# Optimization experiments

Measured on AMD Instinct MI355X. Metric: run time of the kernel, lower is better.

Reference implementation:

```python
import jax, jax.numpy as jnp
import numpy as np

B, T, D = 4, 2048, 1024
H = 16            # n_heads
DH = D // H       # head dim
E = 8             # n_micro_experts
DE = 256          # micro_expert_dim
TOP_K = 2
EPS = 1e-5


def _ln(x, g, b):
    m = jnp.mean(x, axis=-1, keepdims=True)
    v = jnp.mean(jnp.square(x - m), axis=-1, keepdims=True)
    return (x - m) * jax.lax.rsqrt(v + EPS) * g + b


def setup_inputs() -> dict:
    key = jax.random.key(0)
    ks = jax.random.split(key, 12)
    s = 0.02
    return {
        "x": jax.random.normal(ks[0], (B, T, D), dtype=jnp.float32),
        "ln1_g": jnp.ones((D,), jnp.float32),
        "ln1_b": jnp.zeros((D,), jnp.float32),
        "in_proj_w": jax.random.normal(ks[1], (3 * D, D), jnp.float32) * s,
        "in_proj_b": jnp.zeros((3 * D,), jnp.float32),
        "out_proj_w": jax.random.normal(ks[2], (D, D), jnp.float32) * s,
        "out_proj_b": jnp.zeros((D,), jnp.float32),
        "ln2_g": jnp.ones((D,), jnp.float32),
        "ln2_b": jnp.zeros((D,), jnp.float32),
        "router_w": jax.random.normal(ks[3], (E, D), jnp.float32) * s,
        "log_temp": jnp.zeros((), jnp.float32),
        "Wg": jax.random.normal(ks[4], (E, DE, D), jnp.float32) * s,  # gate proj per expert
        "Wu": jax.random.normal(ks[5], (E, DE, D), jnp.float32) * s,  # up proj per expert
        "Wd": jax.random.normal(ks[6], (E, D, DE), jnp.float32) * s,  # down proj per expert
    }


def reference(x, ln1_g, ln1_b, in_proj_w, in_proj_b, out_proj_w, out_proj_b,
              ln2_g, ln2_b, router_w, log_temp, Wg, Wu, Wd):
    # --- self-attention block (nn.MultiheadAttention, batch_first, no mask) ---
    h = _ln(x, ln1_g, ln1_b)
    qkv = h @ in_proj_w.T + in_proj_b                       # [B,T,3D]
    q, k, v = jnp.split(qkv, 3, axis=-1)
    q = q.reshape(B, T, H, DH).transpose(0, 2, 1, 3)        # [B,H,T,DH]
    k = k.reshape(B, T, H, DH).transpose(0, 2, 1, 3)
    v = v.reshape(B, T, H, DH).transpose(0, 2, 1, 3)
    scores = jnp.einsum("bhqd,bhkd->bhqk", q, k) / np.sqrt(DH).astype(np.float32)
    attn = jax.nn.softmax(scores, axis=-1)
    o = jnp.einsum("bhqk,bhkd->bhqd", attn, v)              # [B,H,T,DH]
    o = o.transpose(0, 2, 1, 3).reshape(B, T, D)
    x = x + o @ out_proj_w.T + out_proj_b

    # --- MicroExpert MoE (soft top-k via sigmoid suppression, dense experts) ---
    h2 = _ln(x, ln2_g, ln2_b)
    temp = jax.nn.softplus(log_temp) + 0.1
    logits = (h2 @ router_w.T) / temp                       # [B,T,E]
    top_vals, _ = jax.lax.top_k(logits, TOP_K)
    threshold = jax.lax.stop_gradient(top_vals[..., -1:])   # k-th largest, detached
    suppression = jax.nn.sigmoid(10.0 * (logits - threshold))
    weights = jax.nn.softmax(logits * suppression, axis=-1)  # [B,T,E]

    hg = jnp.einsum("btd,efd->btef", h2, Wg)                # [B,T,E,DE]
    hu = jnp.einsum("btd,efd->btef", h2, Wu)
    act = jax.nn.silu(hg) * hu
    out_e = jnp.einsum("btef,edf->bted", act, Wd)           # [B,T,E,D]
    moe = jnp.einsum("bted,bte->btd", out_e, weights)
    return x + moe
```

## Files before the change

kernel.cpp:

```cpp
#include <hip/hip_runtime.h>
#include <hip/hip_bf16.h>
#include <cstddef>
#include <cstdint>

constexpr int Bc  = 4;
constexpr int Tc  = 2048;
constexpr int Dc  = 1024;
constexpr int Hc  = 16;
constexpr int Ec  = 8;
constexpr int DEc = 256;
constexpr int NTOK = Bc * Tc;
constexpr int EDE = Ec * DEc;

typedef __attribute__((ext_vector_type(8)))  short  s8v;
typedef __attribute__((ext_vector_type(4)))  float  f4v;
typedef __attribute__((ext_vector_type(16))) float  f16v;
typedef __attribute__((ext_vector_type(8)))  ushort u8v;
typedef __attribute__((ext_vector_type(4)))  ushort u4v;

constexpr float LOG2E = 1.44269504088896340736f;

__device__ inline ushort f2bf(float f) {
  union { float f; uint32_t u; } v; v.f = f;
  uint32_t r = v.u + 0x7FFFu + ((v.u >> 16) & 1u);
  return (ushort)(r >> 16);
}
__device__ inline float exp2v(float x) {
  float r; asm("v_exp_f32 %0, %1" : "=v"(r) : "v"(x)); return r;
}
__device__ inline float max3f(float a, float b, float c) {
  return fmaxf(fmaxf(a, b), c);
}
__device__ inline float pmax32(float x) {
  float a = x, b = x;
  asm("v_permlane32_swap_b32 %0, %1" : "+v"(b), "+v"(a));
  return fmaxf(a, b);
}
__device__ inline float psum32(float x) {
  float a = x, b = x;
  asm("v_permlane32_swap_b32 %0, %1" : "+v"(b), "+v"(a));
  return a + b;
}

#define GLOAD_LDS(gsrc, ldst)                                        \
  __builtin_amdgcn_global_load_lds(                                  \
      (const __attribute__((address_space(1))) void*)(gsrc),         \
      (__attribute__((address_space(3))) void*)(ldst), 16, 0, 0)

__device__ inline uint32_t cvtpk(float a, float b) {
  uint32_t r;
  asm("v_cvt_pk_bf16_f32 %0, %1, %2" : "=v"(r) : "v"(a), "v"(b));
  return r;
}

__device__ inline u8v pack8(const float4& a, const float4& b) {
  u8v o;
  o[0] = f2bf(a.x); o[1] = f2bf(a.y); o[2] = f2bf(a.z); o[3] = f2bf(a.w);
  o[4] = f2bf(b.x); o[5] = f2bf(b.y); o[6] = f2bf(b.z); o[7] = f2bf(b.w);
  return o;
}

__global__ __launch_bounds__(256)
void convert_all(const float* __restrict__ in_w, const float* __restrict__ out_w,
                 const float* __restrict__ Wg, const float* __restrict__ Wu,
                 const float* __restrict__ Wd,
                 ushort* __restrict__ wb_in, ushort* __restrict__ wb_out,
                 ushort* __restrict__ wb_gu, ushort* __restrict__ wb_d) {
  const int b = blockIdx.x;
  const int tid = threadIdx.x;
  if (b < 1536) {
    const size_t i = ((size_t)b * 256 + tid) * 8;
    *(u8v*)(wb_in + i) = pack8(*(const float4*)(in_w + i),
                               *(const float4*)(in_w + i + 4));
  } else if (b < 2048) {
    const size_t i = ((size_t)(b - 1536) * 256 + tid) * 8;
    *(u8v*)(wb_out + i) = pack8(*(const float4*)(out_w + i),
                                *(const float4*)(out_w + i + 4));
  } else if (b < 4096) {
    const size_t i = ((size_t)(b - 2048) * 256 + tid) * 8;
    const int r = (int)(i >> 10), k = (int)(i & 1023);
    const int j = ((r >> 5) << 4) + (r & 15);
    const float* src = (r & 16) ? Wu : Wg;
    *(u8v*)(wb_gu + i) = pack8(*(const float4*)(src + (size_t)j * Dc + k),
                               *(const float4*)(src + (size_t)j * Dc + k + 4));
  } else {
    const size_t i = ((size_t)(b - 4096) * 256 + tid) * 8;
    const int e = (int)(i >> 18);
    const int d = (int)((i >> 8) & 1023);
    const int f = (int)(i & 255);
    *(u8v*)(wb_d + (size_t)d * EDE + e * DEc + f) =
        pack8(*(const float4*)(Wd + i), *(const float4*)(Wd + i + 4));
  }
}

template <int ROUTER>
__global__ __launch_bounds__(256)
void ln_kernel(const float* __restrict__ in, const float* __restrict__ g,
               const float* __restrict__ bt, ushort* __restrict__ out,
               const float* __restrict__ rw, const float* __restrict__ log_temp,
               float* __restrict__ wts) {
  const int row = blockIdx.x;
  const int tid = threadIdx.x;
  const float* xr = in + (size_t)row * Dc;
  float4 v = *(const float4*)(xr + tid * 4);
  float s  = v.x + v.y + v.z + v.w;
  float ss = v.x * v.x + v.y * v.y + v.z * v.z + v.w * v.w;
#pragma unroll
  for (int off = 32; off; off >>= 1) {
    s  += __shfl_xor(s, off);
    ss += __shfl_xor(ss, off);
  }
  __shared__ float red[8];
  const int w = tid >> 6;
  if ((tid & 63) == 0) { red[w] = s; red[4 + w] = ss; }
  __syncthreads();
  const float ts  = red[0] + red[1] + red[2] + red[3];
  const float tss = red[4] + red[5] + red[6] + red[7];
  const float mean = ts * (1.0f / Dc);
  const float var  = tss * (1.0f / Dc) - mean * mean;
  const float rstd = rsqrtf(var + 1e-5f);
  float4 gv = *(const float4*)(g + tid * 4);
  float4 bv = *(const float4*)(bt + tid * 4);
  const float n0 = (v.x - mean) * rstd * gv.x + bv.x;
  const float n1 = (v.y - mean) * rstd * gv.y + bv.y;
  const float n2 = (v.z - mean) * rstd * gv.z + bv.z;
  const float n3 = (v.w - mean) * rstd * gv.w + bv.w;
  u4v o;
  o[0] = f2bf(n0); o[1] = f2bf(n1); o[2] = f2bf(n2); o[3] = f2bf(n3);
  *(u4v*)(out + (size_t)row * Dc + tid * 4) = o;
  if constexpr (ROUTER) {
    float part[Ec];
#pragma unroll
    for (int e = 0; e < Ec; ++e) {
      float4 wv = *(const float4*)(rw + (size_t)e * Dc + tid * 4);
      part[e] = n0 * wv.x + n1 * wv.y + n2 * wv.z + n3 * wv.w;
    }
#pragma unroll
    for (int off = 32; off; off >>= 1) {
#pragma unroll
      for (int e = 0; e < Ec; ++e) part[e] += __shfl_xor(part[e], off);
    }
    __shared__ float red2[4][Ec];
    if ((tid & 63) == 0) {
#pragma unroll
      for (int e = 0; e < Ec; ++e) red2[w][e] = part[e];
    }
    __syncthreads();
    if (tid == 0) {
      const float lt = *log_temp;
      const float temp = log1pf(__expf(lt)) + 0.1f;
      float lg[Ec];
#pragma unroll
      for (int e = 0; e < Ec; ++e)
        lg[e] = (red2[0][e] + red2[1][e] + red2[2][e] + red2[3][e]) / temp;
      float m1 = -1e30f, m2 = -1e30f;
#pragma unroll
      for (int e = 0; e < Ec; ++e) {
        const float vv = lg[e];
        if (vv > m1) { m2 = m1; m1 = vv; }
        else if (vv > m2) { m2 = vv; }
      }
      float sl[Ec];
      float mx = -1e30f;
#pragma unroll
      for (int e = 0; e < Ec; ++e) {
        const float sup = 1.f / (1.f + __expf(-10.f * (lg[e] - m2)));
        sl[e] = lg[e] * sup;
        mx = fmaxf(mx, sl[e]);
      }
      float ssum = 0.f;
#pragma unroll
      for (int e = 0; e < Ec; ++e) {
        const float p = __expf(sl[e] - mx);
        sl[e] = p;
        ssum += p;
      }
      const float inv = 1.f / ssum;
#pragma unroll
      for (int e = 0; e < Ec; ++e) wts[(size_t)row * Ec + e] = sl[e] * inv;
    }
  }
}

template <int EPI>
__global__ __launch_bounds__(512, 2)
void gemm256(const ushort* __restrict__ A, int lda,
             const ushort* __restrict__ B,
             const float* __restrict__ bias,
             void* __restrict__ Cout, int K) {
  __shared__ __align__(16) ushort Asm[2][256 * 64];
  __shared__ __align__(16) ushort Bsm[2][256 * 64];
  const int tid = threadIdx.x;
  const int lane = tid & 63, w = tid >> 6;
  const int g = lane >> 4, c = lane & 15;
  const int wr = w >> 2, wc = w & 3;
  int bid = blockIdx.y * gridDim.x + blockIdx.x;
  const int qq = (gridDim.x * gridDim.y) >> 3;
  bid = (bid & 7) * qq + (bid >> 3);
  const int m0 = (bid / gridDim.x) * 256, n0 = (bid % gridDim.x) * 256;
  f4v acc[8][4];
#pragma unroll
  for (int i = 0; i < 8; ++i)
#pragma unroll
    for (int j = 0; j < 4; ++j) acc[i][j] = f4v{0.f, 0.f, 0.f, 0.f};

  const int srow = tid >> 3;
  const int koff = 8 * ((tid & 7) ^ (srow & 7));

#define STAGE_A(buf, kt, i)                                                  \
  GLOAD_LDS(A + (size_t)(m0 + (i) * 64 + srow) * lda + (kt) * 64 + koff,     \
            &Asm[buf][((i) * 512 + tid) * 8])
#define STAGE_B(buf, kt, i)                                                  \
  GLOAD_LDS(B + (size_t)(n0 + (i) * 64 + srow) * K + (kt) * 64 + koff,       \
            &Bsm[buf][((i) * 512 + tid) * 8])

#define RD_A(buf, mi, ks)                                                    \
  (*(const s8v*)&Asm[buf][(wr * 128 + (mi) * 16 + c) * 64 +                  \
      8 * (((ks) * 4 + g) ^ ((wr * 128 + (mi) * 16 + c) & 7))])
#define RD_B(buf, ni, ks)                                                    \
  (*(const s8v*)&Bsm[buf][(wc * 64 + (ni) * 16 + c) * 64 +                   \
      8 * (((ks) * 4 + g) ^ ((wc * 64 + (ni) * 16 + c) & 7))])

  const int NT = K >> 6;
  STAGE_B(0, 0, 0); STAGE_B(0, 0, 1); STAGE_B(0, 0, 2); STAGE_B(0, 0, 3);
  STAGE_A(0, 0, 0); STAGE_A(0, 0, 2); STAGE_A(0, 0, 1); STAGE_A(0, 0, 3);
  asm volatile("s_waitcnt vmcnt(0)" ::: "memory");
  __builtin_amdgcn_s_barrier();

  for (int t = 0; t < NT; ++t) {
    const int cur = t & 1, nxt = cur ^ 1;
    const bool st = (t + 1 < NT);
    s8v bf[2][4], af[2][2];
#pragma unroll
    for (int ks = 0; ks < 2; ++ks) {
#pragma unroll
      for (int ni = 0; ni < 4; ++ni) bf[ks][ni] = RD_B(cur, ni, ks);
      af[ks][0] = RD_A(cur, 0, ks); af[ks][1] = RD_A(cur, 1, ks);
    }
    if (st) { STAGE_B(nxt, t + 1, 0); STAGE_B(nxt, t + 1, 1); }
    __builtin_amdgcn_s_barrier();
    __builtin_amdgcn_s_setprio(1);
#pragma unroll
    for (int ks = 0; ks < 2; ++ks)
#pragma unroll
      for (int q = 0; q < 2; ++q)
#pragma unroll
        for (int ni = 0; ni < 4; ++ni)
          acc[q][ni] = __builtin_amdgcn_mfma_f32_16x16x32_bf16(
              af[ks][q], bf[ks][ni], acc[q][ni], 0, 0, 0);
    __builtin_amdgcn_s_setprio(0);
    __builtin_amdgcn_s_barrier();
#pragma unroll
    for (int ks = 0; ks < 2; ++ks) {
      af[ks][0] = RD_A(cur, 2, ks); af[ks][1] = RD_A(cur, 3, ks);
    }
    if (st) { STAGE_B(nxt, t + 1, 2); STAGE_B(nxt, t + 1, 3); }
    __builtin_amdgcn_s_barrier();
    __builtin_amdgcn_s_setprio(1);
#pragma unroll
    for (int ks = 0; ks < 2; ++ks)
#pragma unroll
      for (int q = 0; q < 2; ++q)
#pragma unroll
        for (int ni = 0; ni < 4; ++ni)
          acc[2 + q][ni] = __builtin_amdgcn_mfma_f32_16x16x32_bf16(
              af[ks][q], bf[ks][ni], acc[2 + q][ni], 0, 0, 0);
    __builtin_amdgcn_s_setprio(0);
    if (st) asm volatile("s_waitcnt vmcnt(4)" ::: "memory");
    else    asm volatile("s_waitcnt vmcnt(0)" ::: "memory");
    __builtin_amdgcn_s_barrier();
#pragma unroll
    for (int ks = 0; ks < 2; ++ks) {
      af[ks][0] = RD_A(cur, 4, ks); af[ks][1] = RD_A(cur, 5, ks);
    }
    if (st) { STAGE_A(nxt, t + 1, 0); STAGE_A(nxt, t + 1, 2); }
    __builtin_amdgcn_s_barrier();
    __builtin_amdgcn_s_setprio(1);
#pragma unroll
    for (int ks = 0; ks < 2; ++ks)
#pragma unroll
      for (int q = 0; q < 2; ++q)
#pragma unroll
        for (int ni = 0; ni < 4; ++ni)
          acc[4 + q][ni] = __builtin_amdgcn_mfma_f32_16x16x32_bf16(
              af[ks][q], bf[ks][ni], acc[4 + q][ni], 0, 0, 0);
    __builtin_amdgcn_s_setprio(0);
    __builtin_amdgcn_s_barrier();
#pragma unroll
    for (int ks = 0; ks < 2; ++ks) {
      af[ks][0] = RD_A(cur, 6, ks); af[ks][1] = RD_A(cur, 7, ks);
    }
    if (st) { STAGE_A(nxt, t + 1, 1); STAGE_A(nxt, t + 1, 3); }
    __builtin_amdgcn_s_barrier();
    __builtin_amdgcn_s_setprio(1);
#pragma unroll
    for (int ks = 0; ks < 2; ++ks)
#pragma unroll
      for (int q = 0; q < 2; ++q)
#pragma unroll
        for (int ni = 0; ni < 4; ++ni)
          acc[6 + q][ni] = __builtin_amdgcn_mfma_f32_16x16x32_bf16(
              af[ks][q], bf[ks][ni], acc[6 + q][ni], 0, 0, 0);
    __builtin_amdgcn_s_setprio(0);
    if (st) asm volatile("s_waitcnt vmcnt(2)" ::: "memory");
    __builtin_amdgcn_s_barrier();
  }
#undef STAGE_A
#undef STAGE_B
#undef RD_A
#undef RD_B

#pragma unroll
  for (int mi = 0; mi < 8; ++mi) {
    if constexpr (EPI == 4) {
#pragma unroll
      for (int nip = 0; nip < 2; ++nip) {
        const int jbase = ((n0 + wc * 64) >> 1) + nip * 16;
        const int e = jbase >> 8;
#pragma unroll
        for (int j = 0; j < 4; ++j) {
          const int row = m0 + wr * 128 + mi * 16 + g * 4 + j;
          const float wgt = bias[(size_t)row * Ec + e];
          const float gv = acc[mi][2 * nip][j];
          const float uv = acc[mi][2 * nip + 1][j];
          const float av = (gv / (1.f + __expf(-gv))) * uv * wgt;
          ((ushort*)Cout)[(size_t)row * EDE + jbase + c] = f2bf(av);
        }
      }
    } else {
#pragma unroll
      for (int ni = 0; ni < 4; ++ni) {
        const int col = n0 + wc * 64 + ni * 16 + c;
        const int which = col >> 10, hh = (col >> 6) & 15, d = col & 63;
        const int row0 = m0 + wr * 128 + mi * 16 + g * 4;
        const int b = row0 >> 11, t0 = row0 & 2047;
        const float bs = bias[col];
        ushort* base = (ushort*)Cout;
        if (which == 2) {
          u4v pk;
#pragma unroll
          for (int j = 0; j < 4; ++j) pk[j] = f2bf(acc[mi][ni][j] + bs);
          *(u4v*)&base[2 * (size_t)NTOK * Dc +
                       (((size_t)(b * Hc + hh)) * 64 + d) * Tc + t0] = pk;
        } else {
          const float qs = (which == 0) ? 0.125f * LOG2E : 1.f;
          const size_t off = (size_t)which * ((size_t)NTOK * Dc);
#pragma unroll
          for (int j = 0; j < 4; ++j)
            base[off + (((size_t)(b * Hc + hh)) * Tc + t0 + j) * 64 + d] =
                f2bf((acc[mi][ni][j] + bs) * qs);
        }
      }
    }
  }
}

template <int EPI>
__global__ __launch_bounds__(256)
void gemm_bf16(const ushort* __restrict__ A, int lda,
               const ushort* __restrict__ B,
               const float* __restrict__ bias, const float* __restrict__ resid,
               void* __restrict__ Cout, int ldc, int K) {
  __shared__ __align__(16) ushort As[2][128 * 64];
  __shared__ __align__(16) ushort Bs[2][128 * 64];
  const int tid = threadIdx.x;
  const int lane = tid & 63, w = tid >> 6;
  const int g = lane >> 4, c = lane & 15;
  int bid = blockIdx.y * gridDim.x + blockIdx.x;
  const int qq = (gridDim.x * gridDim.y) >> 3;
  bid = (bid & 7) * qq + (bid >> 3);
  const int m0 = (bid / gridDim.x) * 128, n0 = (bid % gridDim.x) * 128;
  const int wm = (w >> 1) * 64, wn = (w & 1) * 64;
  f4v acc[4][4];
#pragma unroll
  for (int i = 0; i < 4; ++i)
#pragma unroll
    for (int j = 0; j < 4; ++j) acc[i][j] = f4v{0.f, 0.f, 0.f, 0.f};

  const int srow = tid >> 3;
  const int koff = ((tid & 7) * 8) ^ ((srow & 7) << 3);
  auto stage = [&](int buf, int k0) {
#pragma unroll
    for (int seg = 0; seg < 4; ++seg) {
      const int r = seg * 32 + srow;
      GLOAD_LDS(A + (size_t)(m0 + r) * lda + k0 + koff,
                &As[buf][(seg * 256 + tid) * 8]);
      GLOAD_LDS(B + (size_t)(n0 + r) * K + k0 + koff,
                &Bs[buf][(seg * 256 + tid) * 8]);
    }
  };

  stage(0, 0);
  int curb = 0;
  for (int k0 = 0; k0 < K; k0 += 64) {
    const bool st = (k0 + 64 < K);
    if (st) {
      stage(curb ^ 1, k0 + 64);
      asm volatile("s_waitcnt vmcnt(8)" ::: "memory");
    } else {
      asm volatile("s_waitcnt vmcnt(0)" ::: "memory");
    }
    __builtin_amdgcn_s_barrier();
    s8v af[2][4], bf[2][4];
#pragma unroll
    for (int ks = 0; ks < 2; ++ks) {
#pragma unroll
      for (int mi = 0; mi < 4; ++mi) {
        const int R = wm + mi * 16 + c;
        af[ks][mi] = *(const s8v*)&As[curb][R * 64 + 8 * ((ks * 4 + g) ^ (R & 7))];
      }
#pragma unroll
      for (int ni = 0; ni < 4; ++ni) {
        const int R = wn + ni * 16 + c;
        bf[ks][ni] = *(const s8v*)&Bs[curb][R * 64 + 8 * ((ks * 4 + g) ^ (R & 7))];
      }
    }
    __builtin_amdgcn_s_setprio(1);
#pragma unroll
    for (int ks = 0; ks < 2; ++ks)
#pragma unroll
      for (int mi = 0; mi < 4; ++mi)
#pragma unroll
        for (int ni = 0; ni < 4; ++ni)
          acc[mi][ni] = __builtin_amdgcn_mfma_f32_16x16x32_bf16(
              af[ks][mi], bf[ks][ni], acc[mi][ni], 0, 0, 0);
    __builtin_amdgcn_s_setprio(0);
    __builtin_amdgcn_s_barrier();
    curb ^= 1;
  }

#pragma unroll
  for (int mi = 0; mi < 4; ++mi) {
#pragma unroll
    for (int ni = 0; ni < 4; ++ni) {
#pragma unroll
      for (int j = 0; j < 4; ++j) {
        const int row = m0 + wm + mi * 16 + g * 4 + j;
        const int col = n0 + wn + ni * 16 + c;
        float v = acc[mi][ni][j];
        if constexpr (EPI == 1) {
          v += bias[col] + resid[(size_t)row * ldc + col];
          ((float*)Cout)[(size_t)row * ldc + col] = v;
        } else {
          ((float*)Cout)[(size_t)row * ldc + col] += v;
        }
      }
    }
  }
}

__global__ __launch_bounds__(512)
void attn_mfma(const ushort* __restrict__ Qb, const ushort* __restrict__ Kb,
               const ushort* __restrict__ Vt, ushort* __restrict__ Ob) {
  __shared__ __align__(16) ushort Ksm[2][64 * 64];
  __shared__ __align__(16) ushort Vtsm[2][64 * 64];
  const int tid = threadIdx.x;
  const int lane = tid & 63, w = tid >> 6;
  const int ql = lane & 31, hi = lane >> 5;
  int bid = blockIdx.x;
  bid = (bid & 7) * 64 + (bid >> 3);
  const int qt = bid & 7, bh = bid >> 3;
  const ushort* Qh = Qb + (size_t)bh * Tc * 64;
  const ushort* Kh = Kb + (size_t)bh * Tc * 64;
  const ushort* Vth = Vt + (size_t)bh * 64 * Tc;
  const int qrow = qt * 256 + w * 32 + ql;
  s8v qf[4];
#pragma unroll
  for (int ds = 0; ds < 4; ++ds)
    qf[ds] = *(const s8v*)(Qh + (size_t)qrow * 64 + ds * 16 + hi * 8);
  f16v accO0, accO1;
#pragma unroll
  for (int i = 0; i < 16; ++i) { accO0[i] = 0.f; accO1[i] = 0.f; }
  float mold = -1e30f, lsum = 0.f;
  const int srow = tid >> 3;
  const int soff = ((tid & 7) * 8) ^ ((srow & 7) << 3);
  auto stage = [&](int buf, int j0) {
    GLOAD_LDS(Kh + (size_t)(j0 + srow) * 64 + soff, &Ksm[buf][tid * 8]);
    GLOAD_LDS(Vth + (size_t)srow * Tc + j0 + soff, &Vtsm[buf][tid * 8]);
  };

  stage(0, 0);
  int cur = 0;
  for (int j0 = 0; j0 < Tc; j0 += 64) {
    const bool st = (j0 + 64 < Tc);
    if (st) {
      stage(cur ^ 1, j0 + 64);
      asm volatile("s_waitcnt vmcnt(2)" ::: "memory");
    } else {
      asm volatile("s_waitcnt vmcnt(0)" ::: "memory");
    }
    __builtin_amdgcn_s_barrier();
    f16v s0, s1;
#pragma unroll
    for (int i = 0; i < 16; ++i) { s0[i] = 0.f; s1[i] = 0.f; }
    __builtin_amdgcn_s_setprio(1);
#pragma unroll
    for (int ds = 0; ds < 4; ++ds) {
      const int col = (ds * 16 + hi * 8);
      const int r0 = ql;
      s8v kf0 = *(const s8v*)&Ksm[cur][r0 * 64 + (col ^ ((r0 & 7) << 3))];
      s0 = __builtin_amdgcn_mfma_f32_32x32x16_bf16(kf0, qf[ds], s0, 0, 0, 0);
      const int r1 = 32 + ql;
      s8v kf1 = *(const s8v*)&Ksm[cur][r1 * 64 + (col ^ ((r1 & 7) << 3))];
      s1 = __builtin_amdgcn_mfma_f32_32x32x16_bf16(kf1, qf[ds], s1, 0, 0, 0);
    }
    __builtin_amdgcn_s_setprio(0);
    float cc0 = fmaxf(s0[0], s1[0]), cc1 = fmaxf(s0[1], s1[1]);
    float cc2 = fmaxf(s0[2], s1[2]), cc3 = fmaxf(s0[3], s1[3]);
#pragma unroll
    for (int i = 4; i < 16; i += 4) {
      cc0 = max3f(cc0, s0[i + 0], s1[i + 0]);
      cc1 = max3f(cc1, s0[i + 1], s1[i + 1]);
      cc2 = max3f(cc2, s0[i + 2], s1[i + 2]);
      cc3 = max3f(cc3, s0[i + 3], s1[i + 3]);
    }
    float mx = pmax32(fmaxf(max3f(cc0, cc1, cc2), cc3));
    const bool need = mx > mold + 11.5416f;
    if (__any((int)need)) {
      const float mnew = fmaxf(mold, mx);
      const float sc = exp2v(mold - mnew);
      lsum *= sc;
#pragma unroll
      for (int i = 0; i < 16; ++i) { accO0[i] *= sc; accO1[i] *= sc; }
      mold = mnew;
    }
    float r0s = 0.f, r1s = 0.f, r2s = 0.f, r3s = 0.f;
#pragma unroll
    for (int i = 0; i < 16; i += 4) {
      s0[i+0] = exp2v(s0[i+0] - mold); r0s += s0[i+0];
      s0[i+1] = exp2v(s0[i+1] - mold); r1s += s0[i+1];
      s0[i+2] = exp2v(s0[i+2] - mold); r2s += s0[i+2];
      s0[i+3] = exp2v(s0[i+3] - mold); r3s += s0[i+3];
      s1[i+0] = exp2v(s1[i+0] - mold); r0s += s1[i+0];
      s1[i+1] = exp2v(s1[i+1] - mold); r1s += s1[i+1];
      s1[i+2] = exp2v(s1[i+2] - mold); r2s += s1[i+2];
      s1[i+3] = exp2v(s1[i+3] - mold); r3s += s1[i+3];
    }
    lsum += psum32((r0s + r1s) + (r2s + r3s));
    s8v pa[4];
#pragma unroll
    for (int s = 0; s < 4; ++s) {
      const f16v st2 = (s < 2) ? s0 : s1;
      const int mA = 2 * (s & 1);
      uint32_t a0 = cvtpk(st2[4 * mA + 0], st2[4 * mA + 1]);
      uint32_t a1 = cvtpk(st2[4 * mA + 2], st2[4 * mA + 3]);
      uint32_t b0 = cvtpk(st2[4 * mA + 4], st2[4 * mA + 5]);
      uint32_t b1 = cvtpk(st2[4 * mA + 6], st2[4 * mA + 7]);
      asm("v_permlane32_swap_b32 %0, %1" : "+v"(b0), "+v"(a0));
      asm("v_permlane32_swap_b32 %0, %1" : "+v"(b1), "+v"(a1));
      union { uint32_t u[4]; s8v v; } pk;
      pk.u[0] = a0; pk.u[1] = a1; pk.u[2] = b0; pk.u[3] = b1;
      pa[s] = pk.v;
    }
    __builtin_amdgcn_s_setprio(1);
#pragma unroll
    for (int s = 0; s < 4; ++s) {
      const int col = (s * 16 + hi * 8);
      const int r0 = ql;
      s8v vf0 = *(const s8v*)&Vtsm[cur][r0 * 64 + (col ^ ((r0 & 7) << 3))];
      accO0 = __builtin_amdgcn_mfma_f32_32x32x16_bf16(vf0, pa[s], accO0, 0, 0, 0);
      const int r1 = 32 + ql;
      s8v vf1 = *(const s8v*)&Vtsm[cur][r1 * 64 + (col ^ ((r1 & 7) << 3))];
      accO1 = __builtin_amdgcn_mfma_f32_32x32x16_bf16(vf1, pa[s], accO1, 0, 0, 0);
    }
    __builtin_amdgcn_s_setprio(0);
    __builtin_amdgcn_s_barrier();
    cur ^= 1;
  }
  const int h = bh & 15, b = bh >> 4;
  const int tok = b * Tc + qt * 256 + w * 32 + ql;
  const float inv = 1.f / lsum;
  ushort* orow = Ob + (size_t)tok * Dc + h * 64;
#pragma unroll
  for (int dt = 0; dt < 2; ++dt) {
    const f16v ac = dt ? accO1 : accO0;
#pragma unroll
    for (int rq = 0; rq < 4; ++rq) {
      u4v pk;
#pragma unroll
      for (int j = 0; j < 4; ++j) pk[j] = f2bf(ac[4 * rq + j] * inv);
      *(u4v*)&orow[dt * 32 + 8 * rq + 4 * hi] = pk;
    }
  }
}

extern "C" void kernel_launch(void* const* d_in, const int* in_sizes, int n_in,
                              void* d_out, int out_size, void* d_ws, size_t ws_size,
                              hipStream_t stream) {
  (void)in_sizes; (void)n_in; (void)out_size; (void)ws_size;
  const float* x        = (const float*)d_in[0];
  const float* ln1_g    = (const float*)d_in[1];
  const float* ln1_b    = (const float*)d_in[2];
  const float* in_w     = (const float*)d_in[3];
  const float* in_b     = (const float*)d_in[4];
  const float* out_w    = (const float*)d_in[5];
  const float* out_b    = (const float*)d_in[6];
  const float* ln2_g    = (const float*)d_in[7];
  const float* ln2_b    = (const float*)d_in[8];
  const float* rw       = (const float*)d_in[9];
  const float* log_temp = (const float*)d_in[10];
  const float* Wg       = (const float*)d_in[11];
  const float* Wu       = (const float*)d_in[12];
  const float* Wd       = (const float*)d_in[13];
  float* out = (float*)d_out;

  ushort* h_bf   = (ushort*)d_ws;
  ushort* Qb     = h_bf   + (size_t)NTOK * Dc;
  ushort* Kb     = Qb     + (size_t)NTOK * Dc;
  ushort* Vt     = Kb     + (size_t)NTOK * Dc;
  ushort* Ob     = Vt     + (size_t)NTOK * Dc;
  ushort* act    = Ob     + (size_t)NTOK * Dc;
  ushort* wb_in  = act    + (size_t)NTOK * EDE;
  ushort* wb_out = wb_in  + (size_t)3 * Dc * Dc;
  ushort* wb_gu  = wb_out + (size_t)Dc * Dc;
  ushort* wb_d   = wb_gu  + (size_t)2 * EDE * Dc;
  float*  wts    = (float*)(wb_d + (size_t)Dc * EDE);

  const dim3 blk(256);

  convert_all<<<dim3(5120), blk, 0, stream>>>(
      in_w, out_w, Wg, Wu, Wd, wb_in, wb_out, wb_gu, wb_d);

  ln_kernel<0><<<dim3(NTOK), blk, 0, stream>>>(x, ln1_g, ln1_b, h_bf,
                                               nullptr, nullptr, nullptr);
  gemm256<0><<<dim3(3 * Dc / 256, NTOK / 256), dim3(512), 0, stream>>>(
      h_bf, Dc, wb_in, in_b, Qb, Dc);
  attn_mfma<<<dim3(Bc * Hc * (Tc / 256)), dim3(512), 0, stream>>>(
      Qb, Kb, Vt, Ob);
  gemm_bf16<1><<<dim3(Dc / 128, NTOK / 128), blk, 0, stream>>>(
      Ob, Dc, wb_out, out_b, x, out, Dc, Dc);
  ln_kernel<1><<<dim3(NTOK), blk, 0, stream>>>(out, ln2_g, ln2_b, h_bf,
                                               rw, log_temp, wts);
  gemm256<4><<<dim3(2 * EDE / 256, NTOK / 256), dim3(512), 0, stream>>>(
      h_bf, Dc, wb_gu, wts, act, Dc);
  gemm_bf16<3><<<dim3(Dc / 128, NTOK / 128), blk, 0, stream>>>(
      act, EDE, wb_d, nullptr, nullptr, out, Dc, EDE);
}
```

Baseline: 366.3 us.

## Fuse LN1 into weight-convert kernel and deepen attention K/V pipeline to 128-key chunks

The first layernorm is folded into the weight-conversion launch as extra blocks, which removes one kernel launch and lets the two run concurrently. The attention kernel moves from a 2-buffer, 64-key staging scheme to 4 LDS buffers. Two 64-key tiles are now processed between barriers, with the next two prefetched ahead. This halves the number of barriers and is meant to hide more global-load latency. The cost is doubled LDS per block (64KB), which may reduce occupancy.

```diff
diff --git a/kernel.cpp b/kernel.cpp
--- a/kernel.cpp
+++ b/kernel.cpp
@@ -65,7 +65,9 @@
                  const float* __restrict__ Wg, const float* __restrict__ Wu,
                  const float* __restrict__ Wd,
                  ushort* __restrict__ wb_in, ushort* __restrict__ wb_out,
-                 ushort* __restrict__ wb_gu, ushort* __restrict__ wb_d) {
+                 ushort* __restrict__ wb_gu, ushort* __restrict__ wb_d,
+                 const float* __restrict__ x, const float* __restrict__ ln1_g,
+                 const float* __restrict__ ln1_b, ushort* __restrict__ h_bf) {
   const int b = blockIdx.x;
   const int tid = threadIdx.x;
   if (b < 1536) {
@@ -83,13 +85,41 @@
     const float* src = (r & 16) ? Wu : Wg;
     *(u8v*)(wb_gu + i) = pack8(*(const float4*)(src + (size_t)j * Dc + k),
                                *(const float4*)(src + (size_t)j * Dc + k + 4));
-  } else {
+  } else if (b < 5120) {
     const size_t i = ((size_t)(b - 4096) * 256 + tid) * 8;
     const int e = (int)(i >> 18);
     const int d = (int)((i >> 8) & 1023);
     const int f = (int)(i & 255);
     *(u8v*)(wb_d + (size_t)d * EDE + e * DEc + f) =
         pack8(*(const float4*)(Wd + i), *(const float4*)(Wd + i + 4));
+  } else {
+    const int row = b - 5120;
+    const float* xr = x + (size_t)row * Dc;
+    float4 v = *(const float4*)(xr + tid * 4);
+    float s  = v.x + v.y + v.z + v.w;
+    float ss = v.x * v.x + v.y * v.y + v.z * v.z + v.w * v.w;
+#pragma unroll
+    for (int off = 32; off; off >>= 1) {
+      s  += __shfl_xor(s, off);
+      ss += __shfl_xor(ss, off);
+    }
+    __shared__ float red[8];
+    const int w = tid >> 6;
+    if ((tid & 63) == 0) { red[w] = s; red[4 + w] = ss; }
+    __syncthreads();
+    const float ts  = red[0] + red[1] + red[2] + red[3];
+    const float tss = red[4] + red[5] + red[6] + red[7];
+    const float mean = ts * (1.0f / Dc);
+    const float var  = tss * (1.0f / Dc) - mean * mean;
+    const float rstd = rsqrtf(var + 1e-5f);
+    float4 gv = *(const float4*)(ln1_g + tid * 4);
+    float4 bv = *(const float4*)(ln1_b + tid * 4);
+    u4v o;
+    o[0] = f2bf((v.x - mean) * rstd * gv.x + bv.x);
+    o[1] = f2bf((v.y - mean) * rstd * gv.y + bv.y);
+    o[2] = f2bf((v.z - mean) * rstd * gv.z + bv.z);
+    o[3] = f2bf((v.w - mean) * rstd * gv.w + bv.w);
+    *(u4v*)(h_bf + (size_t)row * Dc + tid * 4) = o;
   }
 }
 
@@ -452,8 +482,8 @@
 __global__ __launch_bounds__(512)
 void attn_mfma(const ushort* __restrict__ Qb, const ushort* __restrict__ Kb,
                const ushort* __restrict__ Vt, ushort* __restrict__ Ob) {
-  __shared__ __align__(16) ushort Ksm[2][64 * 64];
-  __shared__ __align__(16) ushort Vtsm[2][64 * 64];
+  __shared__ __align__(16) ushort Ksm[4][64 * 64];
+  __shared__ __align__(16) ushort Vtsm[4][64 * 64];
   const int tid = threadIdx.x;
   const int lane = tid & 63, w = tid >> 6;
   const int ql = lane & 31, hi = lane >> 5;
@@ -478,18 +508,7 @@
     GLOAD_LDS(Kh + (size_t)(j0 + srow) * 64 + soff, &Ksm[buf][tid * 8]);
     GLOAD_LDS(Vth + (size_t)srow * Tc + j0 + soff, &Vtsm[buf][tid * 8]);
   };
-
-  stage(0, 0);
-  int cur = 0;
-  for (int j0 = 0; j0 < Tc; j0 += 64) {
-    const bool st = (j0 + 64 < Tc);
-    if (st) {
-      stage(cur ^ 1, j0 + 64);
-      asm volatile("s_waitcnt vmcnt(2)" ::: "memory");
-    } else {
-      asm volatile("s_waitcnt vmcnt(0)" ::: "memory");
-    }
-    __builtin_amdgcn_s_barrier();
+  auto chunk = [&](int buf) {
     f16v s0, s1;
 #pragma unroll
     for (int i = 0; i < 16; ++i) { s0[i] = 0.f; s1[i] = 0.f; }
@@ -498,10 +517,10 @@
     for (int ds = 0; ds < 4; ++ds) {
       const int col = (ds * 16 + hi * 8);
       const int r0 = ql;
-      s8v kf0 = *(const s8v*)&Ksm[cur][r0 * 64 + (col ^ ((r0 & 7) << 3))];
+      s8v kf0 = *(const s8v*)&Ksm[buf][r0 * 64 + (col ^ ((r0 & 7) << 3))];
       s0 = __builtin_amdgcn_mfma_f32_32x32x16_bf16(kf0, qf[ds], s0, 0, 0, 0);
       const int r1 = 32 + ql;
-      s8v kf1 = *(const s8v*)&Ksm[cur][r1 * 64 + (col ^ ((r1 & 7) << 3))];
+      s8v kf1 = *(const s8v*)&Ksm[buf][r1 * 64 + (col ^ ((r1 & 7) << 3))];
       s1 = __builtin_amdgcn_mfma_f32_32x32x16_bf16(kf1, qf[ds], s1, 0, 0, 0);
     }
     __builtin_amdgcn_s_setprio(0);
@@ -557,15 +576,31 @@
     for (int s = 0; s < 4; ++s) {
       const int col = (s * 16 + hi * 8);
       const int r0 = ql;
-      s8v vf0 = *(const s8v*)&Vtsm[cur][r0 * 64 + (col ^ ((r0 & 7) << 3))];
+      s8v vf0 = *(const s8v*)&Vtsm[buf][r0 * 64 + (col ^ ((r0 & 7) << 3))];
       accO0 = __builtin_amdgcn_mfma_f32_32x32x16_bf16(vf0, pa[s], accO0, 0, 0, 0);
       const int r1 = 32 + ql;
-      s8v vf1 = *(const s8v*)&Vtsm[cur][r1 * 64 + (col ^ ((r1 & 7) << 3))];
+      s8v vf1 = *(const s8v*)&Vtsm[buf][r1 * 64 + (col ^ ((r1 & 7) << 3))];
       accO1 = __builtin_amdgcn_mfma_f32_32x32x16_bf16(vf1, pa[s], accO1, 0, 0, 0);
     }
     __builtin_amdgcn_s_setprio(0);
-    __builtin_amdgcn_s_barrier();
-    cur ^= 1;
+  };
+
+  constexpr int NU = Tc / 128;
+  stage(0, 0);
+  stage(1, 64);
+  for (int u = 0; u < NU; ++u) {
+    const bool st = (u + 1 < NU);
+    if (st) {
+      stage((2 * u + 2) & 3, (2 * u + 2) * 64);
+      stage((2 * u + 3) & 3, (2 * u + 3) * 64);
+      asm volatile("s_waitcnt vmcnt(4)" ::: "memory");
+    } else {
+      asm volatile("s_waitcnt vmcnt(0)" ::: "memory");
+    }
+    __builtin_amdgcn_s_barrier();
+    chunk((2 * u) & 3);
+    chunk((2 * u + 1) & 3);
+    __builtin_amdgcn_s_barrier();
   }
   const int h = bh & 15, b = bh >> 4;
   const int tok = b * Tc + qt * 256 + w * 32 + ql;
@@ -618,11 +653,10 @@
 
   const dim3 blk(256);
 
-  convert_all<<<dim3(5120), blk, 0, stream>>>(
-      in_w, out_w, Wg, Wu, Wd, wb_in, wb_out, wb_gu, wb_d);
-
-  ln_kernel<0><<<dim3(NTOK), blk, 0, stream>>>(x, ln1_g, ln1_b, h_bf,
-                                               nullptr, nullptr, nullptr);
+  convert_all<<<dim3(5120 + NTOK), blk, 0, stream>>>(
+      in_w, out_w, Wg, Wu, Wd, wb_in, wb_out, wb_gu, wb_d,
+      x, ln1_g, ln1_b, h_bf);
+
   gemm256<0><<<dim3(3 * Dc / 256, NTOK / 256), dim3(512), 0, stream>>>(
       h_bf, Dc, wb_in, in_b, Qb, Dc);
   attn_mfma<<<dim3(Bc * Hc * (Tc / 256)), dim3(512), 0, stream>>>(
```

After: 363.7 us. No clear change (-0.7%).
